# Performance work log

Measured on AMD Instinct MI355X. Metric: run time of the kernel, lower is better.

The kernel has to match this reference:

```python
import jax, jax.numpy as jnp
import numpy as np

N_NODES = 10000
N_EDGES = 160000
N_GRAPHS = 64
IN_DIM, HID, HEADS, OUT_DIM = 128, 64, 8, 10
NEG_SLOPE = 0.2


def setup_inputs() -> dict:
    key = jax.random.key(0)
    ks = jax.random.split(key, 20)
    x = jax.random.normal(ks[0], (N_NODES, IN_DIM), dtype=jnp.float32)
    edge_index = jax.random.randint(ks[1], (2, N_EDGES), 0, N_NODES, dtype=jnp.int64)
    batch = jnp.sort(jax.random.randint(ks[2], (N_NODES,), 0, N_GRAPHS, dtype=jnp.int64))

    def glorot(k, shape):
        fan_in, fan_out = shape[0], shape[-1]
        lim = jnp.sqrt(6.0 / (fan_in + fan_out)).astype(jnp.float32)
        return jax.random.uniform(k, shape, jnp.float32, -lim, lim)

    d0 = HID * HEADS  # 512
    params = {
        # layer 0: IN_DIM -> HID x HEADS, concat
        'W0': glorot(ks[3], (IN_DIM, HEADS * HID)),
        'asrc0': glorot(ks[4], (HEADS, HID)), 'adst0': glorot(ks[5], (HEADS, HID)),
        'b0': jnp.zeros((HEADS * HID,), jnp.float32),
        # layer 1: 512 -> HID x HEADS, concat
        'W1': glorot(ks[6], (d0, HEADS * HID)),
        'asrc1': glorot(ks[7], (HEADS, HID)), 'adst1': glorot(ks[8], (HEADS, HID)),
        'b1': jnp.zeros((HEADS * HID,), jnp.float32),
        # layer 2: 512 -> HID, heads=1
        'W2': glorot(ks[9], (d0, HID)),
        'asrc2': glorot(ks[10], (1, HID)), 'adst2': glorot(ks[11], (1, HID)),
        'b2': jnp.zeros((HID,), jnp.float32),
        # classifier: 2*HID -> HID -> OUT_DIM
        'cW1': glorot(ks[12], (2 * HID, HID)), 'cb1': jnp.zeros((HID,), jnp.float32),
        'cW2': glorot(ks[13], (HID, OUT_DIM)), 'cb2': jnp.zeros((OUT_DIM,), jnp.float32),
    }
    return {'x': x, 'edge_index': edge_index, 'batch': batch, **params}


def gat_conv(h_in, src, dst, W, a_src, a_dst, b, heads, ch):
    # PyG GATConv (concat=True, negative_slope=0.2), dropout inactive (eval).
    N = h_in.shape[0]
    h = (h_in @ W).reshape(N, heads, ch)                       # [N,H,C]
    a_s = jnp.sum(h * a_src[None], axis=-1)                    # [N,H]
    a_d = jnp.sum(h * a_dst[None], axis=-1)                    # [N,H]
    e = jax.nn.leaky_relu(a_s[src] + a_d[dst], NEG_SLOPE)      # [E,H]
    # per-destination segment softmax (stable)
    m = jax.ops.segment_max(e, dst, num_segments=N)            # [N,H]
    ex = jnp.exp(e - m[dst])
    s = jax.ops.segment_sum(ex, dst, num_segments=N)
    alpha = ex / (s[dst] + 1e-16)                              # [E,H]
    out = jax.ops.segment_sum(h[src] * alpha[:, :, None], dst, num_segments=N)
    return out.reshape(N, heads * ch) + b


def _forward(x, src, dst, batch,
             W0, asrc0, adst0, b0, W1, asrc1, adst1, b1,
             W2, asrc2, adst2, b2, cW1, cb1, cW2, cb2):
    h = gat_conv(x, src, dst, W0, asrc0, adst0, b0, HEADS, HID)
    h = jax.nn.relu(h)
    h = gat_conv(h, src, dst, W1, asrc1, adst1, b1, HEADS, HID)
    h = jax.nn.relu(h)
    h = gat_conv(h, src, dst, W2, asrc2, adst2, b2, 1, HID)    # [N,HID]
    # global mean + max pool over graphs
    sums = jax.ops.segment_sum(h, batch, num_segments=N_GRAPHS)
    cnt = jax.ops.segment_sum(jnp.ones((h.shape[0], 1), h.dtype), batch, num_segments=N_GRAPHS)
    mean = sums / jnp.maximum(cnt, 1.0)
    mx = jax.ops.segment_max(h, batch, num_segments=N_GRAPHS)
    g = jnp.concatenate([mean, mx], axis=1)                    # [G, 2*HID]
    g = jax.nn.relu(g @ cW1 + cb1)
    return g @ cW2 + cb2                                       # [G, OUT_DIM]


def reference(x, edge_index, batch,
              W0, asrc0, adst0, b0, W1, asrc1, adst1, b1,
              W2, asrc2, adst2, b2, cW1, cb1, cW2, cb2):
    # PyG GATConv adds self-loops by default
    loops = jnp.arange(x.shape[0], dtype=edge_index.dtype)
    src = jnp.concatenate([edge_index[0], loops])
    dst = jnp.concatenate([edge_index[1], loops])
    return _forward(x, src, dst, batch,
                    W0, asrc0, adst0, b0, W1, asrc1, adst1, b1,
                    W2, asrc2, adst2, b2, cW1, cb1, cW2, cb2)
```

## Files before the change

kernel.cpp:

```cpp
#include <hip/hip_runtime.h>
#include <hip/hip_bf16.h>
#include <math.h>

#define NN 10000
#define EIN 160000
#define ETOT 170000
#define NG 64
#define INDIM 128
#define HID 64
#define HEADS 8
#define D0 512
#define OUTD 10

#define GBN 128
#define GBK 32
#define LPAD 8

using bfrag = __attribute__((ext_vector_type(8))) short;
using ffrag = __attribute__((ext_vector_type(4))) float;
using u32x4 = __attribute__((ext_vector_type(4))) unsigned int;

__device__ inline float bf2f(unsigned short u) { return __uint_as_float(((unsigned)u) << 16); }
__device__ inline unsigned short f2bf(float f) {
    __hip_bfloat16 b = __float2bfloat16(f);
    return *reinterpret_cast<unsigned short*>(&b);
}

__device__ void transpose_tile(const float* __restrict__ src, __hip_bfloat16* __restrict__ dst,
                               int R, int C, int bx, int by) {
    __shared__ float tile[32][33];
    int cb = bx * 32, rb = by * 32;
    int tx = threadIdx.x & 31, ty = threadIdx.x >> 5;
#pragma unroll
    for (int i = 0; i < 32; i += 8) {
        int r = rb + ty + i, c = cb + tx;
        tile[ty + i][tx] = (r < R && c < C) ? src[(size_t)r * C + c] : 0.f;
    }
    __syncthreads();
#pragma unroll
    for (int i = 0; i < 32; i += 8) {
        int c = cb + ty + i, r = rb + tx;
        if (c < C && r < R) dst[(size_t)c * R + r] = __float2bfloat16(tile[tx][ty + i]);
    }
}

__global__ __launch_bounds__(256) void prep_kernel(const float* __restrict__ x,
                                                   const float* __restrict__ W0,
                                                   const float* __restrict__ W1,
                                                   const float* __restrict__ W2,
                                                   __hip_bfloat16* __restrict__ xb,
                                                   __hip_bfloat16* __restrict__ W0T,
                                                   __hip_bfloat16* __restrict__ W1T,
                                                   __hip_bfloat16* __restrict__ W2T,
                                                   int* __restrict__ cnt) {
    int bid = blockIdx.x;
    if (bid < 5000) {
        int i = bid * 256 + threadIdx.x;
        xb[i] = __float2bfloat16(x[i]);
    } else if (bid < 5064) {
        int lb = bid - 5000;
        transpose_tile(W0, W0T, INDIM, D0, lb & 15, lb >> 4);
    } else if (bid < 5320) {
        int lb = bid - 5064;
        transpose_tile(W1, W1T, D0, D0, lb & 15, lb >> 4);
    } else if (bid < 5352) {
        int lb = bid - 5320;
        transpose_tile(W2, W2T, D0, 64, lb & 1, lb >> 1);
    } else {
        int i = (bid - 5352) * 256 + threadIdx.x;
        if (i < NN) cnt[i] = 0;
    }
}

__global__ void count_kernel(const int* __restrict__ ei, int* __restrict__ cnt) {
    int i = blockIdx.x * 256 + threadIdx.x;
    if (i >= ETOT) return;
    int dst = (i < EIN) ? ei[EIN + i] : (i - EIN);
    atomicAdd(&cnt[dst], 1);
}

__global__ __launch_bounds__(1024) void scan_kernel(const int* __restrict__ cnt,
                                                    int* __restrict__ row_ptr,
                                                    int* __restrict__ cursor) {
    __shared__ int ssum[1024];
    int t = threadIdx.x;
    const int PER = 10;
    int base = t * PER;
    int loc[PER];
    int s = 0;
#pragma unroll
    for (int i = 0; i < PER; i++) {
        int v = (base + i < NN) ? cnt[base + i] : 0;
        loc[i] = s; s += v;
    }
    ssum[t] = s;
    __syncthreads();
    for (int off = 1; off < 1024; off <<= 1) {
        int v = (t >= off) ? ssum[t - off] : 0;
        __syncthreads();
        ssum[t] += v;
        __syncthreads();
    }
    int bs = (t > 0) ? ssum[t - 1] : 0;
#pragma unroll
    for (int i = 0; i < PER; i++) {
        if (base + i < NN) { int v = bs + loc[i]; row_ptr[base + i] = v; cursor[base + i] = v; }
    }
    if (t == 0) row_ptr[NN] = ssum[1023];
}

__global__ void scatter_kernel(const int* __restrict__ ei, int* __restrict__ cursor,
                               int* __restrict__ col_src) {
    int i = blockIdx.x * 256 + threadIdx.x;
    if (i >= ETOT) return;
    int src, dst;
    if (i < EIN) { src = ei[i]; dst = ei[EIN + i]; }
    else { src = i - EIN; dst = src; }
    int pos = atomicAdd(&cursor[dst], 1);
    col_src[pos] = src;
}

template <int FM>
__global__ __launch_bounds__(256) void gemm_attn(const __hip_bfloat16* __restrict__ A,
                                                 const __hip_bfloat16* __restrict__ BT,
                                                 float* __restrict__ C,
                                                 __hip_bfloat16* __restrict__ Cb,
                                                 const float* __restrict__ asrc,
                                                 const float* __restrict__ adst,
                                                 float* __restrict__ a_s,
                                                 float* __restrict__ a_d,
                                                 int H, int M, int N, int K) {
    constexpr int TM = 32 * FM;
    __shared__ __align__(16) short As[TM][GBK + LPAD];
    __shared__ __align__(16) short Bs[GBN][GBK + LPAD];
    int tid = threadIdx.x;
    int wid = tid >> 6, lane = tid & 63;
    int wr = wid >> 1, wc = wid & 1;
    int brow = blockIdx.y * TM, bcol = blockIdx.x * GBN;

    ffrag acc[FM][4] = {};

    int srow = tid >> 2;
    int skq  = (tid & 3) * 8;

    int kq = (lane >> 4) * 8;
    int ra = lane & 15;

    for (int k0 = 0; k0 < K; k0 += GBK) {
#pragma unroll
        for (int p = 0; p < FM / 2; ++p) {
            int r = srow + p * 64;
            int gr = brow + r;
            bfrag va = {0,0,0,0,0,0,0,0};
            if (gr < M) va = *(const bfrag*)(A + (size_t)gr * K + k0 + skq);
            *(bfrag*)&As[r][skq] = va;
        }
#pragma unroll
        for (int p = 0; p < 2; ++p) {
            int r = srow + p * 64;
            int gc = bcol + r;
            bfrag vb = {0,0,0,0,0,0,0,0};
            if (gc < N) vb = *(const bfrag*)(BT + (size_t)gc * K + k0 + skq);
            *(bfrag*)&Bs[r][skq] = vb;
        }
        __syncthreads();
        bfrag af[FM], bf[4];
#pragma unroll
        for (int m = 0; m < FM; ++m) af[m] = *(const bfrag*)&As[wr * (16 * FM) + m * 16 + ra][kq];
#pragma unroll
        for (int n = 0; n < 4; ++n) bf[n] = *(const bfrag*)&Bs[wc * 64 + n * 16 + ra][kq];
#pragma unroll
        for (int m = 0; m < FM; ++m)
#pragma unroll
            for (int n = 0; n < 4; ++n)
                acc[m][n] = __builtin_amdgcn_mfma_f32_16x16x32_bf16(af[m], bf[n], acc[m][n], 0, 0, 0);
        __syncthreads();
    }

    int cr = (lane >> 4) * 4;
    int cc = lane & 15;

#pragma unroll
    for (int m = 0; m < FM; ++m) {
#pragma unroll
        for (int n = 0; n < 4; ++n) {
#pragma unroll
            for (int r = 0; r < 4; ++r) {
                int grow = brow + wr * (16 * FM) + m * 16 + cr + r;
                int gcol = bcol + wc * 64 + n * 16 + cc;
                if (grow < M && gcol < N) {
                    float v = acc[m][n][r];
                    if (C)  C[(size_t)grow * N + gcol] = v;
                    if (Cb) Cb[(size_t)grow * N + gcol] = __float2bfloat16(v);
                }
            }
        }
    }

    int head = (bcol >> 6) + wc;
    if (head < H) {
        float asl[4], adl[4];
        int cbase = head * 64;
#pragma unroll
        for (int n = 0; n < 4; ++n) {
            asl[n] = asrc[cbase + n * 16 + cc];
            adl[n] = adst[cbase + n * 16 + cc];
        }
#pragma unroll
        for (int m = 0; m < FM; ++m) {
#pragma unroll
            for (int r = 0; r < 4; ++r) {
                float ps = 0.f, pd = 0.f;
#pragma unroll
                for (int n = 0; n < 4; ++n) {
                    float av = acc[m][n][r];
                    ps += av * asl[n];
                    pd += av * adl[n];
                }
#pragma unroll
                for (int o = 1; o < 16; o <<= 1) {
                    ps += __shfl_xor(ps, o);
                    pd += __shfl_xor(pd, o);
                }
                if (cc == 0) {
                    int row = brow + wr * (16 * FM) + m * 16 + cr + r;
                    if (row < M) {
                        a_s[(size_t)row * H + head] = ps;
                        a_d[(size_t)row * H + head] = pd;
                    }
                }
            }
        }
    }
}

__global__ __launch_bounds__(256) void gat_agg8(const __hip_bfloat16* __restrict__ h,
                                                const float* __restrict__ a_s,
                                                const float* __restrict__ a_d,
                                                const int* __restrict__ row_ptr,
                                                const int* __restrict__ col_src,
                                                const float* __restrict__ bias,
                                                __hip_bfloat16* __restrict__ out)
{
    int n = blockIdx.x * 4 + (threadIdx.x >> 6);
    int lane = threadIdx.x & 63;
    int r0 = row_ptr[n], r1 = row_ptr[n + 1];

    int head_c = lane & 7;
    int hme = lane >> 3;
    float ad_c = a_d[n * 8 + head_c];

    float acc[8] = {};
    float ss = 0.f;
    const unsigned short* hu = (const unsigned short*)h;

    int k = r0 + (lane >> 3);
    int kc = (k < r1) ? k : r1 - 1;
    int s_l = col_src[kc];
    {
        float e = a_s[s_l * 8 + head_c] + ad_c;
        e = e > 0.f ? e : 0.2f * e;
        s_l = s_l;
    }
    float e0 = a_s[s_l * 8 + head_c] + ad_c;
    e0 = e0 > 0.f ? e0 : 0.2f * e0;
    float al_l = (k < r1) ? __expf(e0) : 0.f;

    for (int kb = r0; kb < r1; kb += 8) {
        int s_cur = s_l;
        float al_cur = al_l;
        int kb2 = kb + 8;
        bool more = kb2 < r1;
        int s_n = 0;
        if (more) {
            int k2 = kb2 + (lane >> 3);
            int kc2 = (k2 < r1) ? k2 : r1 - 1;
            s_n = col_src[kc2];
        }
#pragma unroll
        for (int j = 0; j < 8; ++j) {
            int   sj = __shfl(s_cur, j * 8);
            float aj = __shfl(al_cur, j * 8 + hme);
            u32x4 v = *(const u32x4*)(hu + (size_t)sj * 512 + (lane << 3));
#pragma unroll
            for (int q = 0; q < 4; ++q) {
                acc[2 * q]     += aj * bf2f((unsigned short)(v[q] & 0xffff));
                acc[2 * q + 1] += aj * bf2f((unsigned short)(v[q] >> 16));
            }
            ss += aj;
        }
        if (more) {
            int k2 = kb2 + (lane >> 3);
            float e = a_s[s_n * 8 + head_c] + ad_c;
            e = e > 0.f ? e : 0.2f * e;
            al_l = (k2 < r1) ? __expf(e) : 0.f;
            s_l = s_n;
        }
    }

    float inv = 1.f / (ss + 1e-16f);
    float4 b0v = *(const float4*)(bias + lane * 8);
    float4 b1v = *(const float4*)(bias + lane * 8 + 4);
    float ov[8];
    ov[0] = fmaxf(acc[0] * inv + b0v.x, 0.f);
    ov[1] = fmaxf(acc[1] * inv + b0v.y, 0.f);
    ov[2] = fmaxf(acc[2] * inv + b0v.z, 0.f);
    ov[3] = fmaxf(acc[3] * inv + b0v.w, 0.f);
    ov[4] = fmaxf(acc[4] * inv + b1v.x, 0.f);
    ov[5] = fmaxf(acc[5] * inv + b1v.y, 0.f);
    ov[6] = fmaxf(acc[6] * inv + b1v.z, 0.f);
    ov[7] = fmaxf(acc[7] * inv + b1v.w, 0.f);
    u32x4 pk;
#pragma unroll
    for (int q = 0; q < 4; ++q)
        pk[q] = (unsigned)f2bf(ov[2 * q]) | ((unsigned)f2bf(ov[2 * q + 1]) << 16);
    *(u32x4*)((unsigned short*)out + (size_t)n * 512 + (lane << 3)) = pk;
}

__global__ __launch_bounds__(256) void gat_agg1(const float* __restrict__ h,
                                                const float* __restrict__ a_s,
                                                const float* __restrict__ a_d,
                                                const int* __restrict__ row_ptr,
                                                const int* __restrict__ col_src,
                                                const float* __restrict__ bias,
                                                float* __restrict__ out) {
    int n = blockIdx.x * 4 + (threadIdx.x >> 6);
    int lane = threadIdx.x & 63;
    if (n >= NN) return;
    int r0 = row_ptr[n], r1 = row_ptr[n + 1];
    float ad = a_d[n];
    float acc = 0.f, ssum = 0.f;
    for (int k = r0; k < r1; k += 8) {
        int kk[8]; int s[8]; float av[8]; float v[8];
#pragma unroll
        for (int i = 0; i < 8; ++i) kk[i] = (k + i < r1) ? k + i : r1 - 1;
#pragma unroll
        for (int i = 0; i < 8; ++i) s[i] = col_src[kk[i]];
#pragma unroll
        for (int i = 0; i < 8; ++i) av[i] = a_s[s[i]];
#pragma unroll
        for (int i = 0; i < 8; ++i) v[i] = h[(size_t)s[i] * 64 + lane];
#pragma unroll
        for (int i = 0; i < 8; ++i) {
            float e = av[i] + ad;
            e = e > 0.f ? e : 0.2f * e;
            float al = __expf(e);
            al = (k + i < r1) ? al : 0.f;
            acc += al * v[i];
            ssum += al;
        }
    }
    out[(size_t)n * 64 + lane] = acc / (ssum + 1e-16f) + bias[lane];
}

__global__ __launch_bounds__(256) void pool_classify(const float* __restrict__ h,
                                                     const int* __restrict__ batch,
                                                     const float* __restrict__ cW1, const float* __restrict__ cb1,
                                                     const float* __restrict__ cW2, const float* __restrict__ cb2,
                                                     float* __restrict__ out) {
    int g = blockIdx.x;
    int tid = threadIdx.x;
    int lane = tid & 63, w = tid >> 6;

    int lo = 0, hi = NN;
    while (lo < hi) { int mid = (lo + hi) >> 1; if (batch[mid] < g) lo = mid + 1; else hi = mid; }
    int s = lo;
    lo = s; hi = NN;
    while (lo < hi) { int mid = (lo + hi) >> 1; if (batch[mid] < g + 1) lo = mid + 1; else hi = mid; }
    int e = lo;

    float sum = 0.f, mx = -1e30f;
    for (int n = s + w; n < e; n += 4) {
        float v = h[(size_t)n * 64 + lane];
        sum += v; mx = fmaxf(mx, v);
    }
    __shared__ float ssum[4][64], smax[4][64];
    __shared__ float gv[128], c1[64];
    ssum[w][lane] = sum; smax[w][lane] = mx;
    __syncthreads();
    if (tid < 64) {
        float s4 = ssum[0][tid] + ssum[1][tid] + ssum[2][tid] + ssum[3][tid];
        float m4 = fmaxf(fmaxf(smax[0][tid], smax[1][tid]), fmaxf(smax[2][tid], smax[3][tid]));
        int cntv = e - s;
        float c = (float)(cntv > 1 ? cntv : 1);
        gv[tid] = s4 / c;
        gv[64 + tid] = m4;
    }
    __syncthreads();
    if (tid < 64) {
        float acc = cb1[tid];
        for (int k = 0; k < 128; k++) acc += gv[k] * cW1[k * 64 + tid];
        c1[tid] = fmaxf(acc, 0.f);
    }
    __syncthreads();
    if (tid < OUTD) {
        float o = cb2[tid];
        for (int k = 0; k < 64; k++) o += c1[k] * cW2[k * OUTD + tid];
        out[g * OUTD + tid] = o;
    }
}

extern "C" void kernel_launch(void* const* d_in, const int* in_sizes, int n_in,
                              void* d_out, int out_size, void* d_ws, size_t ws_size,
                              hipStream_t stream) {
    const float* x     = (const float*)d_in[0];
    const int*   ei    = (const int*)d_in[1];
    const int*   batch = (const int*)d_in[2];
    const float* W0    = (const float*)d_in[3];
    const float* asrc0 = (const float*)d_in[4];
    const float* adst0 = (const float*)d_in[5];
    const float* b0    = (const float*)d_in[6];
    const float* W1    = (const float*)d_in[7];
    const float* asrc1 = (const float*)d_in[8];
    const float* adst1 = (const float*)d_in[9];
    const float* b1    = (const float*)d_in[10];
    const float* W2    = (const float*)d_in[11];
    const float* asrc2 = (const float*)d_in[12];
    const float* adst2 = (const float*)d_in[13];
    const float* b2    = (const float*)d_in[14];
    const float* cW1   = (const float*)d_in[15];
    const float* cb1   = (const float*)d_in[16];
    const float* cW2   = (const float*)d_in[17];
    const float* cb2   = (const float*)d_in[18];
    float* out = (float*)d_out;

    char* ws = (char*)d_ws;
    size_t off = 0;
    auto alloc = [&](size_t bytes) { void* p = ws + off; off += (bytes + 255) & ~(size_t)255; return p; };
    __hip_bfloat16* bufAb = (__hip_bfloat16*)alloc((size_t)NN * D0 * 2);
    __hip_bfloat16* bufBb = (__hip_bfloat16*)alloc((size_t)NN * D0 * 2);
    float* bufC  = (float*)alloc((size_t)NN * 64 * 4);
    float* bufD  = (float*)alloc((size_t)NN * 64 * 4);
    __hip_bfloat16* xb   = (__hip_bfloat16*)alloc((size_t)NN * INDIM * 2);
    __hip_bfloat16* W0T  = (__hip_bfloat16*)alloc((size_t)D0 * INDIM * 2);
    __hip_bfloat16* W1T  = (__hip_bfloat16*)alloc((size_t)D0 * D0 * 2);
    __hip_bfloat16* W2T  = (__hip_bfloat16*)alloc((size_t)64 * D0 * 2);
    float* a_s     = (float*)alloc((size_t)NN * HEADS * 4);
    float* a_d     = (float*)alloc((size_t)NN * HEADS * 4);
    int*   cnt     = (int*)alloc((size_t)NN * 4);
    int*   row_ptr = (int*)alloc((size_t)(NN + 1) * 4);
    int*   cursor  = (int*)alloc((size_t)NN * 4);
    int*   col_src = (int*)alloc((size_t)(ETOT + 8) * 4);
    (void)ws_size; (void)n_in; (void)in_sizes; (void)out_size;

    prep_kernel<<<5392, 256, 0, stream>>>(x, W0, W1, W2, xb, W0T, W1T, W2T, cnt);

    count_kernel<<<(ETOT + 255) / 256, 256, 0, stream>>>(ei, cnt);
    scan_kernel<<<1, 1024, 0, stream>>>(cnt, row_ptr, cursor);
    scatter_kernel<<<(ETOT + 255) / 256, 256, 0, stream>>>(ei, cursor, col_src);

    dim3 gg8(D0 / GBN, (NN + 63) / 64);
    dim3 gg1(1, (NN + 63) / 64);

    gemm_attn<2><<<gg8, 256, 0, stream>>>(xb, W0T, nullptr, bufAb, asrc0, adst0, a_s, a_d, HEADS, NN, D0, INDIM);
    gat_agg8<<<2500, 256, 0, stream>>>(bufAb, a_s, a_d, row_ptr, col_src, b0, bufBb);

    gemm_attn<2><<<gg8, 256, 0, stream>>>(bufBb, W1T, nullptr, bufAb, asrc1, adst1, a_s, a_d, HEADS, NN, D0, D0);
    gat_agg8<<<2500, 256, 0, stream>>>(bufAb, a_s, a_d, row_ptr, col_src, b1, bufBb);

    gemm_attn<2><<<gg1, 256, 0, stream>>>(bufBb, W2T, bufC, nullptr, asrc2, adst2, a_s, a_d, 1, NN, 64, D0);
    gat_agg1<<<(NN + 3) / 4, 256, 0, stream>>>(bufC, a_s, a_d, row_ptr, col_src, b2, bufD);

    pool_classify<<<NG, 256, 0, stream>>>(bufD, batch, cW1, cb1, cW2, cb2, out);
}
```

Measured before the change: 169.8 us.

## Split GAT aggregation channels into quarters mapped to XCDs for L2 locality

The 8-head aggregation kernel now launches four times as many blocks. Each block handles one 128-channel quarter (two heads) of four nodes instead of all 512 channels. Block indices are remapped so that every XCD only ever gathers its own channel slice of the feature matrix. The aim is to cut the gathered working set each XCD's L2 must hold and to raise parallelism. The cost is that edge index loads and the exp computation are repeated per quarter, and each lane now does narrower 4-byte loads instead of 16-byte vector loads.

Result: no change. 171.8 us (+1.2%).

```diff
diff --git a/kernel.cpp b/kernel.cpp
--- a/kernel.cpp
+++ b/kernel.cpp
@@ -242,26 +242,26 @@
                                                 const float* __restrict__ bias,
                                                 __hip_bfloat16* __restrict__ out)
 {
-    int n = blockIdx.x * 4 + (threadIdx.x >> 6);
+    int b = blockIdx.x;
+    int xcd = b & 7;
+    int q = xcd >> 1;
+    int nb = (b >> 3) * 2 + (xcd & 1);
+    int wid = threadIdx.x >> 6;
     int lane = threadIdx.x & 63;
+    int n = nb * 4 + wid;
     int r0 = row_ptr[n], r1 = row_ptr[n + 1];
 
-    int head_c = lane & 7;
-    int hme = lane >> 3;
+    int hl = lane >> 5;
+    int head_c = 2 * q + (lane & 1);
     float ad_c = a_d[n * 8 + head_c];
-
-    float acc[8] = {};
-    float ss = 0.f;
+    int ch = q * 128 + lane * 2;
+
+    float acc0 = 0.f, acc1 = 0.f, ss = 0.f;
     const unsigned short* hu = (const unsigned short*)h;
 
     int k = r0 + (lane >> 3);
     int kc = (k < r1) ? k : r1 - 1;
     int s_l = col_src[kc];
-    {
-        float e = a_s[s_l * 8 + head_c] + ad_c;
-        e = e > 0.f ? e : 0.2f * e;
-        s_l = s_l;
-    }
     float e0 = a_s[s_l * 8 + head_c] + ad_c;
     e0 = e0 > 0.f ? e0 : 0.2f * e0;
     float al_l = (k < r1) ? __expf(e0) : 0.f;
@@ -280,13 +280,10 @@
 #pragma unroll
         for (int j = 0; j < 8; ++j) {
             int   sj = __shfl(s_cur, j * 8);
-            float aj = __shfl(al_cur, j * 8 + hme);
-            u32x4 v = *(const u32x4*)(hu + (size_t)sj * 512 + (lane << 3));
-#pragma unroll
-            for (int q = 0; q < 4; ++q) {
-                acc[2 * q]     += aj * bf2f((unsigned short)(v[q] & 0xffff));
-                acc[2 * q + 1] += aj * bf2f((unsigned short)(v[q] >> 16));
-            }
+            float aj = __shfl(al_cur, j * 8 + hl);
+            unsigned v = *(const unsigned*)(hu + (size_t)sj * 512 + ch);
+            acc0 += aj * bf2f((unsigned short)(v & 0xffff));
+            acc1 += aj * bf2f((unsigned short)(v >> 16));
             ss += aj;
         }
         if (more) {
@@ -299,22 +296,11 @@
     }
 
     float inv = 1.f / (ss + 1e-16f);
-    float4 b0v = *(const float4*)(bias + lane * 8);
-    float4 b1v = *(const float4*)(bias + lane * 8 + 4);
-    float ov[8];
-    ov[0] = fmaxf(acc[0] * inv + b0v.x, 0.f);
-    ov[1] = fmaxf(acc[1] * inv + b0v.y, 0.f);
-    ov[2] = fmaxf(acc[2] * inv + b0v.z, 0.f);
-    ov[3] = fmaxf(acc[3] * inv + b0v.w, 0.f);
-    ov[4] = fmaxf(acc[4] * inv + b1v.x, 0.f);
-    ov[5] = fmaxf(acc[5] * inv + b1v.y, 0.f);
-    ov[6] = fmaxf(acc[6] * inv + b1v.z, 0.f);
-    ov[7] = fmaxf(acc[7] * inv + b1v.w, 0.f);
-    u32x4 pk;
-#pragma unroll
-    for (int q = 0; q < 4; ++q)
-        pk[q] = (unsigned)f2bf(ov[2 * q]) | ((unsigned)f2bf(ov[2 * q + 1]) << 16);
-    *(u32x4*)((unsigned short*)out + (size_t)n * 512 + (lane << 3)) = pk;
+    float2 bv = *(const float2*)(bias + ch);
+    float o0 = fmaxf(acc0 * inv + bv.x, 0.f);
+    float o1 = fmaxf(acc1 * inv + bv.y, 0.f);
+    unsigned pk = (unsigned)f2bf(o0) | ((unsigned)f2bf(o1) << 16);
+    *(unsigned*)((unsigned short*)out + (size_t)n * 512 + ch) = pk;
 }
 
 __global__ __launch_bounds__(256) void gat_agg1(const float* __restrict__ h,
@@ -453,10 +439,10 @@
     dim3 gg1(1, (NN + 63) / 64);
 
     gemm_attn<2><<<gg8, 256, 0, stream>>>(xb, W0T, nullptr, bufAb, asrc0, adst0, a_s, a_d, HEADS, NN, D0, INDIM);
-    gat_agg8<<<2500, 256, 0, stream>>>(bufAb, a_s, a_d, row_ptr, col_src, b0, bufBb);
+    gat_agg8<<<10000, 256, 0, stream>>>(bufAb, a_s, a_d, row_ptr, col_src, b0, bufBb);
 
     gemm_attn<2><<<gg8, 256, 0, stream>>>(bufBb, W1T, nullptr, bufAb, asrc1, adst1, a_s, a_d, HEADS, NN, D0, D0);
-    gat_agg8<<<2500, 256, 0, stream>>>(bufAb, a_s, a_d, row_ptr, col_src, b1, bufBb);
+    gat_agg8<<<10000, 256, 0, stream>>>(bufAb, a_s, a_d, row_ptr, col_src, b1, bufBb);
 
     gemm_attn<2><<<gg1, 256, 0, stream>>>(bufBb, W2T, bufC, nullptr, asrc2, adst2, a_s, a_d, 1, NN, 64, D0);
     gat_agg1<<<(NN + 3) / 4, 256, 0, stream>>>(bufC, a_s, a_d, row_ptr, col_src, b2, bufD);
```
